# Optimization experiments

Measured on AMD Instinct MI355X. Metric: run time of the kernel, lower is better.

Reference implementation:

```python
import jax, jax.numpy as jnp
import numpy as np

EMBED = 512
HEADS = 8
HEAD_DIM = EMBED // HEADS


def setup_inputs() -> dict:
    key = jax.random.key(0)
    ks = jax.random.split(key, 12)
    B, L, D = 2, 4096, EMBED
    s = 1.0 / np.sqrt(D)  # torch Linear default init range scale (approx, uniform)
    def lin(k):
        kw, kb = jax.random.split(k)
        W = jax.random.uniform(kw, (D, D), jnp.float32, -s, s)
        b = jax.random.uniform(kb, (D,), jnp.float32, -s, s)
        return W, b
    Wq, bq = lin(ks[0])
    Wk, bk = lin(ks[1])
    Wv, bv = lin(ks[2])
    Wo, bo = lin(ks[3])
    query = jax.random.normal(ks[4], (B, L, D), jnp.float32)
    key_t = jax.random.normal(ks[5], (B, L, D), jnp.float32)
    value = jax.random.normal(ks[6], (B, L, D), jnp.float32)
    return {"query": query, "key": key_t, "value": value,
            "Wq": Wq, "bq": bq, "Wk": Wk, "bk": bk,
            "Wv": Wv, "bv": bv, "Wo": Wo, "bo": bo}


def reference(query, key, value, Wq, bq, Wk, bk, Wv, bv, Wo, bo):
    B, L, D = query.shape
    H, Hd = HEADS, HEAD_DIM
    scale = Hd ** -0.5
    # torch nn.Linear: y = x @ W.T + b
    q = (query @ Wq.T + bq).reshape(B, L, H, Hd).transpose(0, 2, 1, 3)   # [B,H,L,Hd]
    k = (key   @ Wk.T + bk).reshape(B, -1, H, Hd).transpose(0, 2, 1, 3)
    v = (value @ Wv.T + bv).reshape(B, -1, H, Hd).transpose(0, 2, 1, 3)
    scores = jnp.einsum('bhqd,bhkd->bhqk', q, k) * scale                  # [B,H,L,L]
    causal = jnp.triu(jnp.ones((L, L), dtype=bool), k=1)                  # True above diag
    neg = jnp.finfo(scores.dtype).min
    scores = jnp.where(causal, neg, scores)
    attn = jax.nn.softmax(scores, axis=-1)
    # dropout is identity in eval mode
    out = jnp.einsum('bhqk,bhkd->bhqd', attn, v)                          # [B,H,L,Hd]
    out = out.transpose(0, 2, 1, 3).reshape(B, L, D)
    return out @ Wo.T + bo, attn
```

## Files before the change

### kernel.cpp

```cpp
#include <hip/hip_runtime.h>
#include <hip/hip_bf16.h>


typedef __attribute__((ext_vector_type(8))) __bf16 bf16x8;
typedef __attribute__((ext_vector_type(4))) __bf16 bf16v4;
typedef __attribute__((ext_vector_type(4))) float f32x4;

constexpr int LL = 4096;
constexpr int DD = 512;
constexpr int HH = 8;
constexpr int HD = 64;
constexpr int BB = 2;
constexpr int BL = BB * LL;
constexpr size_t OUT_ELEMS = (size_t)BB * LL * DD;

static __device__ inline bf16x8 cvt8(const float* p) {
    float4 a = *reinterpret_cast<const float4*>(p);
    float4 b = *reinterpret_cast<const float4*>(p + 4);
    bf16x8 r;
    r[0] = (__bf16)a.x; r[1] = (__bf16)a.y; r[2] = (__bf16)a.z; r[3] = (__bf16)a.w;
    r[4] = (__bf16)b.x; r[5] = (__bf16)b.y; r[6] = (__bf16)b.z; r[7] = (__bf16)b.w;
    return r;
}

static __device__ inline float4 up4(unsigned a, unsigned b) {
    float4 r;
    r.x = __uint_as_float(a << 16);
    r.y = __uint_as_float(a & 0xffff0000u);
    r.z = __uint_as_float(b << 16);
    r.w = __uint_as_float(b & 0xffff0000u);
    return r;
}

__global__ __launch_bounds__(256) void cvt_kernel(
    const float* __restrict__ q, const float* __restrict__ k,
    const float* __restrict__ v, __bf16* __restrict__ o)
{
    constexpr size_t N = (size_t)BL * DD;
    size_t i = ((size_t)blockIdx.x * 256 + threadIdx.x) * 8;
    const float* src = q; size_t j = i;
    if (i >= 2 * N)      { src = v; j = i - 2 * N; }
    else if (i >= N)     { src = k; j = i - N; }
    *reinterpret_cast<bf16x8*>(&o[i]) = cvt8(&src[j]);
}

__global__ __launch_bounds__(256) void qkv_kernel(
    const __bf16* __restrict__ Xb,
    const float* __restrict__ Wq, const float* __restrict__ bq,
    const float* __restrict__ Wk, const float* __restrict__ bk,
    const float* __restrict__ Wv, const float* __restrict__ bv,
    __bf16* __restrict__ Qb, __bf16* __restrict__ Kb, __bf16* __restrict__ Vt)
{
    const int z = blockIdx.z;
    const __bf16* x  = Xb + (size_t)z * BL * DD;
    const float* W   = (z == 0) ? Wq : (z == 1) ? Wk : Wv;
    const float* bia = (z == 0) ? bq : (z == 1) ? bk : bv;

    const int wid = threadIdx.x >> 6;
    const int lane = threadIdx.x & 63;
    const int l15 = lane & 15;
    const int lg  = lane >> 4;

    const int r0 = blockIdx.x * 64;
    const int cb = blockIdx.y;
    const int c0 = cb * 64 + wid * 16;

    f32x4 acc[4] = {};
    for (int k0 = 0; k0 < DD; k0 += 32) {
        bf16x8 bfrag = cvt8(&W[(size_t)(c0 + l15) * DD + k0 + lg * 8]);
#pragma unroll
        for (int mt = 0; mt < 4; ++mt) {
            bf16x8 afrag = *reinterpret_cast<const bf16x8*>(
                &x[(size_t)(r0 + mt * 16 + l15) * DD + k0 + lg * 8]);
            acc[mt] = __builtin_amdgcn_mfma_f32_16x16x32_bf16(afrag, bfrag, acc[mt], 0, 0, 0);
        }
    }

    __shared__ __bf16 T[64][72];
    const float bval = bia[c0 + l15];
#pragma unroll
    for (int mt = 0; mt < 4; ++mt)
#pragma unroll
        for (int i = 0; i < 4; ++i) {
            const float val = acc[mt][i] + bval;
            const int row = mt * 16 + lg * 4 + i;
            const int col = wid * 16 + l15;
            if (z == 2) T[col][row] = (__bf16)val;
            else        T[row][col] = (__bf16)val;
        }
    __syncthreads();

    const int tr  = threadIdx.x >> 2;
    const int seg = threadIdx.x & 3;
    uint4 v0 = *reinterpret_cast<const uint4*>(&T[tr][seg * 16]);
    uint4 v1 = *reinterpret_cast<const uint4*>(&T[tr][seg * 16 + 8]);
    const int b  = r0 >> 12;
    const int l0 = r0 & (LL - 1);
    if (z == 2) {
        __bf16* dst = Vt + ((size_t)(b * HH + cb) * HD + tr) * LL + l0 + seg * 16;
        *reinterpret_cast<uint4*>(dst)     = v0;
        *reinterpret_cast<uint4*>(dst + 8) = v1;
    } else {
        __bf16* base = (z == 0) ? Qb : Kb;
        __bf16* dst = base + ((size_t)(b * HH + cb) * LL + l0 + tr) * HD + seg * 16;
        *reinterpret_cast<uint4*>(dst)     = v0;
        *reinterpret_cast<uint4*>(dst + 8) = v1;
    }
}

__global__ __launch_bounds__(512, 3) void attn_kernel(
    const __bf16* __restrict__ Qb, const __bf16* __restrict__ Kb,
    const __bf16* __restrict__ Vt, __bf16* __restrict__ Ob,
    float* __restrict__ attn_out)
{
    const int bh = blockIdx.x;
    const int qb = 63 - blockIdx.y;

    const int wv   = threadIdx.x >> 6;
    const int wr   = wv & 3;
    const int par  = wv >> 2;
    const int lane = threadIdx.x & 63;
    const int l15  = lane & 15;
    const int lg   = lane >> 4;

    const __bf16* Qh = Qb + (size_t)bh * LL * HD;
    const __bf16* Kh = Kb + (size_t)bh * LL * HD;
    const __bf16* Vh = Vt + (size_t)bh * HD * LL;
    float* A_out = attn_out + (size_t)bh * LL * LL;

    __shared__ __bf16 P[8][16][72];
    __shared__ float rsum[2][64];

    const int q0 = qb * 64 + wr * 16;
    const int qrow = q0 + l15;
    const bf16x8 qf0 = *reinterpret_cast<const bf16x8*>(&Qh[(size_t)(q0 + l15) * HD + lg * 8]);
    const bf16x8 qf1 = *reinterpret_cast<const bf16x8*>(&Qh[(size_t)(q0 + l15) * HD + 32 + lg * 8]);

    const float SC = 0.125f * 1.44269504088896f;

    auto loadK = [&](bf16x8 (&kf)[8], int kb) {
        const __bf16* kp = &Kh[((size_t)kb * 64 + l15) * HD + lg * 8];
#pragma unroll
        for (int kt = 0; kt < 4; ++kt) {
            kf[kt * 2]     = *reinterpret_cast<const bf16x8*>(kp + (size_t)kt * 16 * HD);
            kf[kt * 2 + 1] = *reinterpret_cast<const bf16x8*>(kp + (size_t)kt * 16 * HD + 32);
        }
    };

    float rs = 0.f;
    auto body1 = [&](bf16x8 (&kf)[8], int kb) {
        f32x4 s[4] = {};
#pragma unroll
        for (int kt = 0; kt < 4; ++kt) {
            s[kt] = __builtin_amdgcn_mfma_f32_16x16x32_bf16(kf[kt * 2],     qf0, s[kt], 0, 0, 0);
            s[kt] = __builtin_amdgcn_mfma_f32_16x16x32_bf16(kf[kt * 2 + 1], qf1, s[kt], 0, 0, 0);
        }
        const bool diag = (kb == qb);
#pragma unroll
        for (int kt = 0; kt < 4; ++kt)
#pragma unroll
            for (int i = 0; i < 4; ++i) {
                float e = exp2f(s[kt][i] * SC);
                if (diag && (kb * 64 + kt * 16 + lg * 4 + i) > qrow) e = 0.f;
                rs += e;
            }
    };
    {
        bf16x8 kA[8], kB[8];
        int kb = par;
        bool useA = true;
        if (kb <= qb) loadK(kA, kb);
        for (; kb <= qb; kb += 2) {
            if (useA) { if (kb + 2 <= qb) loadK(kB, kb + 2); body1(kA, kb); }
            else      { if (kb + 2 <= qb) loadK(kA, kb + 2); body1(kB, kb); }
            useA = !useA;
        }
    }
    rs += __shfl_xor(rs, 16, 64);
    rs += __shfl_xor(rs, 32, 64);
    if (lane < 16) rsum[par][wr * 16 + l15] = rs;
    __syncthreads();
    const float llog = -log2f(rsum[0][wr * 16 + l15] + rsum[1][wr * 16 + l15]);

    f32x4 oacc[4] = {};
    const int arow = lane >> 2;
    const int aseg = lane & 3;

    auto body2 = [&](bf16x8 (&kf)[8], int kb) {
        bf16x8 vf[8];
        {
            const __bf16* vp = &Vh[(size_t)l15 * LL + (size_t)kb * 64 + lg * 8];
#pragma unroll
            for (int ht = 0; ht < 4; ++ht) {
                vf[ht * 2]     = *reinterpret_cast<const bf16x8*>(vp + (size_t)ht * 16 * LL);
                vf[ht * 2 + 1] = *reinterpret_cast<const bf16x8*>(vp + (size_t)ht * 16 * LL + 32);
            }
        }
        f32x4 s[4] = {};
#pragma unroll
        for (int kt = 0; kt < 4; ++kt) {
            s[kt] = __builtin_amdgcn_mfma_f32_16x16x32_bf16(kf[kt * 2],     qf0, s[kt], 0, 0, 0);
            s[kt] = __builtin_amdgcn_mfma_f32_16x16x32_bf16(kf[kt * 2 + 1], qf1, s[kt], 0, 0, 0);
        }
        const bool diag = (kb == qb);
#pragma unroll
        for (int kt = 0; kt < 4; ++kt) {
            bf16v4 pk;
#pragma unroll
            for (int i = 0; i < 4; ++i) {
                float e = exp2f(fmaf(s[kt][i], SC, llog));
                if (diag && (kb * 64 + kt * 16 + lg * 4 + i) > qrow) e = 0.f;
                pk[i] = (__bf16)e;
            }
            *reinterpret_cast<bf16v4*>(&P[wv][l15][kt * 16 + lg * 4]) = pk;
        }
        {
            uint4 a0 = *reinterpret_cast<const uint4*>(&P[wv][arow][aseg * 16]);
            uint4 a1 = *reinterpret_cast<const uint4*>(&P[wv][arow][aseg * 16 + 8]);
            float4* dst = reinterpret_cast<float4*>(
                &A_out[(size_t)(q0 + arow) * LL + kb * 64 + aseg * 16]);
            dst[0] = up4(a0.x, a0.y);
            dst[1] = up4(a0.z, a0.w);
            dst[2] = up4(a1.x, a1.y);
            dst[3] = up4(a1.z, a1.w);
        }
        const bf16x8 pa0 = *reinterpret_cast<const bf16x8*>(&P[wv][l15][lg * 8]);
        const bf16x8 pa1 = *reinterpret_cast<const bf16x8*>(&P[wv][l15][32 + lg * 8]);
#pragma unroll
        for (int ht = 0; ht < 4; ++ht) {
            oacc[ht] = __builtin_amdgcn_mfma_f32_16x16x32_bf16(pa0, vf[ht * 2],     oacc[ht], 0, 0, 0);
            oacc[ht] = __builtin_amdgcn_mfma_f32_16x16x32_bf16(pa1, vf[ht * 2 + 1], oacc[ht], 0, 0, 0);
        }
    };
    {
        bf16x8 kA[8], kB[8];
        int kb = par;
        bool useA = true;
        if (kb <= qb) loadK(kA, kb);
        for (; kb <= qb; kb += 2) {
            if (useA) { if (kb + 2 <= qb) loadK(kB, kb + 2); body2(kA, kb); }
            else      { if (kb + 2 <= qb) loadK(kA, kb + 2); body2(kB, kb); }
            useA = !useA;
        }
    }

    if (par == 1) {
#pragma unroll
        for (int ht = 0; ht < 4; ++ht)
#pragma unroll
            for (int i = 0; i < 4; ++i)
                P[wv][lg * 4 + i][ht * 16 + l15] = (__bf16)oacc[ht][i];
    }
    __syncthreads();
    if (par == 0) {
#pragma unroll
        for (int ht = 0; ht < 4; ++ht)
#pragma unroll
            for (int i = 0; i < 4; ++i)
                oacc[ht][i] += (float)P[wv + 4][lg * 4 + i][ht * 16 + l15];
#pragma unroll
        for (int ht = 0; ht < 4; ++ht)
#pragma unroll
            for (int i = 0; i < 4; ++i)
                P[wv][lg * 4 + i][ht * 16 + l15] = (__bf16)oacc[ht][i];
        uint4 o0 = *reinterpret_cast<const uint4*>(&P[wv][arow][aseg * 16]);
        uint4 o1 = *reinterpret_cast<const uint4*>(&P[wv][arow][aseg * 16 + 8]);
        const int b = bh >> 3, h = bh & 7;
        __bf16* dst = Ob + ((size_t)(b * LL + q0 + arow)) * DD + h * HD + aseg * 16;
        *reinterpret_cast<uint4*>(dst)     = o0;
        *reinterpret_cast<uint4*>(dst + 8) = o1;
    }

    {
        const int ztr  = threadIdx.x >> 3;
        const int zseg = threadIdx.x & 7;
        const size_t rowbase = (size_t)(qb * 64 + ztr) * LL;
        const float4 z4 = {0.f, 0.f, 0.f, 0.f};
        for (int c = (qb + 1) * 64 + zseg * 16; c < LL; c += 128) {
            float4* d = reinterpret_cast<float4*>(&A_out[rowbase + c]);
            d[0] = z4; d[1] = z4; d[2] = z4; d[3] = z4;
        }
    }
}

__global__ __launch_bounds__(256) void oproj_kernel(
    const __bf16* __restrict__ Ob, const float* __restrict__ Wo,
    const float* __restrict__ bo, float* __restrict__ out)
{
    const int wid = threadIdx.x >> 6;
    const int lane = threadIdx.x & 63;
    const int l15 = lane & 15;
    const int lg  = lane >> 4;

    const int r0 = blockIdx.x * 64;
    const int c0 = blockIdx.y * 64 + wid * 16;

    f32x4 acc[4] = {};
    for (int k0 = 0; k0 < DD; k0 += 32) {
        bf16x8 bfrag = cvt8(&Wo[(size_t)(c0 + l15) * DD + k0 + lg * 8]);
#pragma unroll
        for (int mt = 0; mt < 4; ++mt) {
            bf16x8 afrag = *reinterpret_cast<const bf16x8*>(
                &Ob[(size_t)(r0 + mt * 16 + l15) * DD + k0 + lg * 8]);
            acc[mt] = __builtin_amdgcn_mfma_f32_16x16x32_bf16(afrag, bfrag, acc[mt], 0, 0, 0);
        }
    }
    const float bval = bo[c0 + l15];
#pragma unroll
    for (int mt = 0; mt < 4; ++mt)
#pragma unroll
        for (int i = 0; i < 4; ++i)
            out[(size_t)(r0 + mt * 16 + lg * 4 + i) * DD + c0 + l15] = acc[mt][i] + bval;
}

extern "C" void kernel_launch(void* const* d_in, const int* in_sizes, int n_in,
                              void* d_out, int out_size, void* d_ws, size_t ws_size,
                              hipStream_t stream) {
    const float* query = (const float*)d_in[0];
    const float* key_t = (const float*)d_in[1];
    const float* value = (const float*)d_in[2];
    const float* Wq = (const float*)d_in[3];
    const float* bq = (const float*)d_in[4];
    const float* Wk = (const float*)d_in[5];
    const float* bk = (const float*)d_in[6];
    const float* Wv = (const float*)d_in[7];
    const float* bv = (const float*)d_in[8];
    const float* Wo = (const float*)d_in[9];
    const float* bo = (const float*)d_in[10];

    float* out  = (float*)d_out;
    float* attn = out + OUT_ELEMS;

    char* ws = (char*)d_ws;
    __bf16* Qb = (__bf16*)(ws);
    __bf16* Kb = (__bf16*)(ws + (size_t)8 * 1024 * 1024);
    __bf16* Vt = (__bf16*)(ws + (size_t)16 * 1024 * 1024);
    __bf16* Ob = (__bf16*)(ws + (size_t)24 * 1024 * 1024);
    __bf16* Xb = (__bf16*)(ws + (size_t)32 * 1024 * 1024);

    cvt_kernel<<<dim3(3 * BL * DD / 8 / 256), 256, 0, stream>>>(query, key_t, value, Xb);
    qkv_kernel<<<dim3(BL / 64, DD / 64, 3), 256, 0, stream>>>(
        Xb, Wq, bq, Wk, bk, Wv, bv, Qb, Kb, Vt);
    attn_kernel<<<dim3(BB * HH, LL / 64), 512, 0, stream>>>(Qb, Kb, Vt, Ob, attn);
    oproj_kernel<<<dim3(BL / 64, DD / 64), 256, 0, stream>>>(Ob, Wo, bo, out);
}
```

Before: 854.0 us.

## Split attention over key chunks into rowsum, main and reduce kernels

Replaces the single attention kernel with a split-K style pipeline. A rowsum kernel computes partial softmax denominators per key chunk, the main kernel computes probabilities and partial P·V per chunk, and a reduce kernel sums the partial outputs. Masked chunks write zeros directly, and attn is now stored from registers in fp32 instead of via bf16 shared memory. The aim is to balance the causal triangle's uneven work across many more blocks. The cost is extra launches, a workspace round trip for partials, and recomputing QK in both passes.

```diff
diff --git a/kernel.cpp b/kernel.cpp
--- a/kernel.cpp
+++ b/kernel.cpp
@@ -13,6 +13,8 @@
 constexpr int BB = 2;
 constexpr int BL = BB * LL;
 constexpr size_t OUT_ELEMS = (size_t)BB * LL * DD;
+constexpr int CH = 16;
+constexpr int NCHUNK = LL / 64 / CH;
 
 static __device__ inline bf16x8 cvt8(const float* p) {
     float4 a = *reinterpret_cast<const float4*>(p);
@@ -20,15 +22,6 @@
     bf16x8 r;
     r[0] = (__bf16)a.x; r[1] = (__bf16)a.y; r[2] = (__bf16)a.z; r[3] = (__bf16)a.w;
     r[4] = (__bf16)b.x; r[5] = (__bf16)b.y; r[6] = (__bf16)b.z; r[7] = (__bf16)b.w;
-    return r;
-}
-
-static __device__ inline float4 up4(unsigned a, unsigned b) {
-    float4 r;
-    r.x = __uint_as_float(a << 16);
-    r.y = __uint_as_float(a & 0xffff0000u);
-    r.z = __uint_as_float(b << 16);
-    r.w = __uint_as_float(b & 0xffff0000u);
     return r;
 }
 
@@ -108,52 +101,40 @@
     }
 }
 
-__global__ __launch_bounds__(512, 3) void attn_kernel(
+__global__ __launch_bounds__(256) void rowsum_kernel(
     const __bf16* __restrict__ Qb, const __bf16* __restrict__ Kb,
-    const __bf16* __restrict__ Vt, __bf16* __restrict__ Ob,
-    float* __restrict__ attn_out)
+    float* __restrict__ rspart)
 {
     const int bh = blockIdx.x;
     const int qb = 63 - blockIdx.y;
+    const int ch = blockIdx.z;
+    if (ch * CH > qb) return;
 
     const int wv   = threadIdx.x >> 6;
-    const int wr   = wv & 3;
-    const int par  = wv >> 2;
     const int lane = threadIdx.x & 63;
     const int l15  = lane & 15;
     const int lg   = lane >> 4;
 
     const __bf16* Qh = Qb + (size_t)bh * LL * HD;
     const __bf16* Kh = Kb + (size_t)bh * LL * HD;
-    const __bf16* Vh = Vt + (size_t)bh * HD * LL;
-    float* A_out = attn_out + (size_t)bh * LL * LL;
-
-    __shared__ __bf16 P[8][16][72];
-    __shared__ float rsum[2][64];
-
-    const int q0 = qb * 64 + wr * 16;
+
+    const int q0 = qb * 64 + wv * 16;
     const int qrow = q0 + l15;
-    const bf16x8 qf0 = *reinterpret_cast<const bf16x8*>(&Qh[(size_t)(q0 + l15) * HD + lg * 8]);
-    const bf16x8 qf1 = *reinterpret_cast<const bf16x8*>(&Qh[(size_t)(q0 + l15) * HD + 32 + lg * 8]);
-
+    const bf16x8 qf0 = *reinterpret_cast<const bf16x8*>(&Qh[(size_t)qrow * HD + lg * 8]);
+    const bf16x8 qf1 = *reinterpret_cast<const bf16x8*>(&Qh[(size_t)qrow * HD + 32 + lg * 8]);
     const float SC = 0.125f * 1.44269504088896f;
 
-    auto loadK = [&](bf16x8 (&kf)[8], int kb) {
-        const __bf16* kp = &Kh[((size_t)kb * 64 + l15) * HD + lg * 8];
+    float rs = 0.f;
+    const int kend = (qb < ch * CH + CH - 1) ? qb : ch * CH + CH - 1;
+    for (int kb = ch * CH; kb <= kend; ++kb) {
+        f32x4 s[4] = {};
 #pragma unroll
         for (int kt = 0; kt < 4; ++kt) {
-            kf[kt * 2]     = *reinterpret_cast<const bf16x8*>(kp + (size_t)kt * 16 * HD);
-            kf[kt * 2 + 1] = *reinterpret_cast<const bf16x8*>(kp + (size_t)kt * 16 * HD + 32);
-        }
-    };
-
-    float rs = 0.f;
-    auto body1 = [&](bf16x8 (&kf)[8], int kb) {
-        f32x4 s[4] = {};
-#pragma unroll
-        for (int kt = 0; kt < 4; ++kt) {
-            s[kt] = __builtin_amdgcn_mfma_f32_16x16x32_bf16(kf[kt * 2],     qf0, s[kt], 0, 0, 0);
-            s[kt] = __builtin_amdgcn_mfma_f32_16x16x32_bf16(kf[kt * 2 + 1], qf1, s[kt], 0, 0, 0);
+            const __bf16* kp = &Kh[(size_t)(kb * 64 + kt * 16 + l15) * HD + lg * 8];
+            const bf16x8 k0 = *reinterpret_cast<const bf16x8*>(kp);
+            const bf16x8 k1 = *reinterpret_cast<const bf16x8*>(kp + 32);
+            s[kt] = __builtin_amdgcn_mfma_f32_16x16x32_bf16(k0, qf0, s[kt], 0, 0, 0);
+            s[kt] = __builtin_amdgcn_mfma_f32_16x16x32_bf16(k1, qf1, s[kt], 0, 0, 0);
         }
         const bool diag = (kb == qb);
 #pragma unroll
@@ -164,31 +145,79 @@
                 if (diag && (kb * 64 + kt * 16 + lg * 4 + i) > qrow) e = 0.f;
                 rs += e;
             }
-    };
-    {
-        bf16x8 kA[8], kB[8];
-        int kb = par;
-        bool useA = true;
-        if (kb <= qb) loadK(kA, kb);
-        for (; kb <= qb; kb += 2) {
-            if (useA) { if (kb + 2 <= qb) loadK(kB, kb + 2); body1(kA, kb); }
-            else      { if (kb + 2 <= qb) loadK(kA, kb + 2); body1(kB, kb); }
-            useA = !useA;
-        }
     }
     rs += __shfl_xor(rs, 16, 64);
     rs += __shfl_xor(rs, 32, 64);
-    if (lane < 16) rsum[par][wr * 16 + l15] = rs;
-    __syncthreads();
-    const float llog = -log2f(rsum[0][wr * 16 + l15] + rsum[1][wr * 16 + l15]);
+    if (lane < 16)
+        rspart[((size_t)bh * LL + qrow) * NCHUNK + ch] = rs;
+}
+
+__global__ __launch_bounds__(256, 4) void attn_main_kernel(
+    const __bf16* __restrict__ Qb, const __bf16* __restrict__ Kb,
+    const __bf16* __restrict__ Vt, const float* __restrict__ rspart,
+    __bf16* __restrict__ opart, float* __restrict__ attn_out)
+{
+    const int bh = blockIdx.x;
+    const int qb = 63 - blockIdx.y;
+    const int ch = blockIdx.z;
+
+    const int wv   = threadIdx.x >> 6;
+    const int lane = threadIdx.x & 63;
+    const int l15  = lane & 15;
+    const int lg   = lane >> 4;
+
+    float* A_out = attn_out + (size_t)bh * LL * LL;
+    const int q0 = qb * 64 + wv * 16;
+    const int qrow = q0 + l15;
+    const int kb0 = ch * CH;
+
+    if (kb0 > qb) {
+        const float4 z4 = {0.f, 0.f, 0.f, 0.f};
+        float4* dst = reinterpret_cast<float4*>(&A_out[(size_t)qrow * LL + kb0 * 64 + lg * 4]);
+        for (int t = 0; t < CH; ++t) {
+#pragma unroll
+            for (int kt = 0; kt < 4; ++kt) dst[kt * 4] = z4;
+            dst += 16;
+        }
+        return;
+    }
+
+    const __bf16* Qh = Qb + (size_t)bh * LL * HD;
+    const __bf16* Kh = Kb + (size_t)bh * LL * HD;
+    const __bf16* Vh = Vt + (size_t)bh * HD * LL;
+
+    __shared__ __bf16 P[4][16][72];
+
+    const bf16x8 qf0 = *reinterpret_cast<const bf16x8*>(&Qh[(size_t)qrow * HD + lg * 8]);
+    const bf16x8 qf1 = *reinterpret_cast<const bf16x8*>(&Qh[(size_t)qrow * HD + 32 + lg * 8]);
+
+    float rsv = 0.f;
+    const int nc = qb >> 4;
+    const float* rp = &rspart[((size_t)bh * LL + qrow) * NCHUNK];
+    for (int c = 0; c <= nc; ++c) rsv += rp[c];
+    const float llog = -log2f(rsv);
+    const float SC = 0.125f * 1.44269504088896f;
 
     f32x4 oacc[4] = {};
-    const int arow = lane >> 2;
-    const int aseg = lane & 3;
-
-    auto body2 = [&](bf16x8 (&kf)[8], int kb) {
-        bf16x8 vf[8];
+
+    for (int t = 0; t < CH; ++t) {
+        const int kb = kb0 + t;
+        if (kb > qb) {
+            const float4 z4 = {0.f, 0.f, 0.f, 0.f};
+            float4* dst = reinterpret_cast<float4*>(
+                &A_out[(size_t)qrow * LL + kb * 64 + lg * 4]);
+#pragma unroll
+            for (int kt = 0; kt < 4; ++kt) dst[kt * 4] = z4;
+            continue;
+        }
+        bf16x8 kf[8], vf[8];
         {
+            const __bf16* kp = &Kh[(size_t)(kb * 64 + l15) * HD + lg * 8];
+#pragma unroll
+            for (int kt = 0; kt < 4; ++kt) {
+                kf[kt * 2]     = *reinterpret_cast<const bf16x8*>(kp + (size_t)kt * 16 * HD);
+                kf[kt * 2 + 1] = *reinterpret_cast<const bf16x8*>(kp + (size_t)kt * 16 * HD + 32);
+            }
             const __bf16* vp = &Vh[(size_t)l15 * LL + (size_t)kb * 64 + lg * 8];
 #pragma unroll
             for (int ht = 0; ht < 4; ++ht) {
@@ -205,24 +234,24 @@
         const bool diag = (kb == qb);
 #pragma unroll
         for (int kt = 0; kt < 4; ++kt) {
+            float e0 = exp2f(fmaf(s[kt][0], SC, llog));
+            float e1 = exp2f(fmaf(s[kt][1], SC, llog));
+            float e2 = exp2f(fmaf(s[kt][2], SC, llog));
+            float e3 = exp2f(fmaf(s[kt][3], SC, llog));
+            if (diag) {
+                const int kc = kb * 64 + kt * 16 + lg * 4;
+                if (kc + 0 > qrow) e0 = 0.f;
+                if (kc + 1 > qrow) e1 = 0.f;
+                if (kc + 2 > qrow) e2 = 0.f;
+                if (kc + 3 > qrow) e3 = 0.f;
+            }
+            float4 ev = {e0, e1, e2, e3};
+            *reinterpret_cast<float4*>(
+                &A_out[(size_t)qrow * LL + kb * 64 + kt * 16 + lg * 4]) = ev;
             bf16v4 pk;
-#pragma unroll
-            for (int i = 0; i < 4; ++i) {
-                float e = exp2f(fmaf(s[kt][i], SC, llog));
-                if (diag && (kb * 64 + kt * 16 + lg * 4 + i) > qrow) e = 0.f;
-                pk[i] = (__bf16)e;
-            }
+            pk[0] = (__bf16)e0; pk[1] = (__bf16)e1;
+            pk[2] = (__bf16)e2; pk[3] = (__bf16)e3;
             *reinterpret_cast<bf16v4*>(&P[wv][l15][kt * 16 + lg * 4]) = pk;
-        }
-        {
-            uint4 a0 = *reinterpret_cast<const uint4*>(&P[wv][arow][aseg * 16]);
-            uint4 a1 = *reinterpret_cast<const uint4*>(&P[wv][arow][aseg * 16 + 8]);
-            float4* dst = reinterpret_cast<float4*>(
-                &A_out[(size_t)(q0 + arow) * LL + kb * 64 + aseg * 16]);
-            dst[0] = up4(a0.x, a0.y);
-            dst[1] = up4(a0.z, a0.w);
-            dst[2] = up4(a1.x, a1.y);
-            dst[3] = up4(a1.z, a1.w);
         }
         const bf16x8 pa0 = *reinterpret_cast<const bf16x8*>(&P[wv][l15][lg * 8]);
         const bf16x8 pa1 = *reinterpret_cast<const bf16x8*>(&P[wv][l15][32 + lg * 8]);
@@ -231,56 +260,49 @@
             oacc[ht] = __builtin_amdgcn_mfma_f32_16x16x32_bf16(pa0, vf[ht * 2],     oacc[ht], 0, 0, 0);
             oacc[ht] = __builtin_amdgcn_mfma_f32_16x16x32_bf16(pa1, vf[ht * 2 + 1], oacc[ht], 0, 0, 0);
         }
-    };
-    {
-        bf16x8 kA[8], kB[8];
-        int kb = par;
-        bool useA = true;
-        if (kb <= qb) loadK(kA, kb);
-        for (; kb <= qb; kb += 2) {
-            if (useA) { if (kb + 2 <= qb) loadK(kB, kb + 2); body2(kA, kb); }
-            else      { if (kb + 2 <= qb) loadK(kA, kb + 2); body2(kB, kb); }
-            useA = !useA;
-        }
-    }
-
-    if (par == 1) {
-#pragma unroll
-        for (int ht = 0; ht < 4; ++ht)
-#pragma unroll
-            for (int i = 0; i < 4; ++i)
-                P[wv][lg * 4 + i][ht * 16 + l15] = (__bf16)oacc[ht][i];
-    }
-    __syncthreads();
-    if (par == 0) {
-#pragma unroll
-        for (int ht = 0; ht < 4; ++ht)
-#pragma unroll
-            for (int i = 0; i < 4; ++i)
-                oacc[ht][i] += (float)P[wv + 4][lg * 4 + i][ht * 16 + l15];
-#pragma unroll
-        for (int ht = 0; ht < 4; ++ht)
-#pragma unroll
-            for (int i = 0; i < 4; ++i)
-                P[wv][lg * 4 + i][ht * 16 + l15] = (__bf16)oacc[ht][i];
-        uint4 o0 = *reinterpret_cast<const uint4*>(&P[wv][arow][aseg * 16]);
-        uint4 o1 = *reinterpret_cast<const uint4*>(&P[wv][arow][aseg * 16 + 8]);
-        const int b = bh >> 3, h = bh & 7;
-        __bf16* dst = Ob + ((size_t)(b * LL + q0 + arow)) * DD + h * HD + aseg * 16;
-        *reinterpret_cast<uint4*>(dst)     = o0;
-        *reinterpret_cast<uint4*>(dst + 8) = o1;
-    }
-
-    {
-        const int ztr  = threadIdx.x >> 3;
-        const int zseg = threadIdx.x & 7;
-        const size_t rowbase = (size_t)(qb * 64 + ztr) * LL;
-        const float4 z4 = {0.f, 0.f, 0.f, 0.f};
-        for (int c = (qb + 1) * 64 + zseg * 16; c < LL; c += 128) {
-            float4* d = reinterpret_cast<float4*>(&A_out[rowbase + c]);
-            d[0] = z4; d[1] = z4; d[2] = z4; d[3] = z4;
-        }
-    }
+    }
+
+#pragma unroll
+    for (int ht = 0; ht < 4; ++ht)
+#pragma unroll
+        for (int i = 0; i < 4; ++i)
+            P[wv][lg * 4 + i][ht * 16 + l15] = (__bf16)oacc[ht][i];
+    const int arow = lane >> 2;
+    const int aseg = lane & 3;
+    uint4 o0 = *reinterpret_cast<const uint4*>(&P[wv][arow][aseg * 16]);
+    uint4 o1 = *reinterpret_cast<const uint4*>(&P[wv][arow][aseg * 16 + 8]);
+    __bf16* dst = opart + ((size_t)((bh * 64 + qb) * NCHUNK + ch)) * 4096
+                + (wv * 16 + arow) * 64 + aseg * 16;
+    *reinterpret_cast<uint4*>(dst)     = o0;
+    *reinterpret_cast<uint4*>(dst + 8) = o1;
+}
+
+__global__ __launch_bounds__(256) void oreduce_kernel(
+    const __bf16* __restrict__ opart, __bf16* __restrict__ Ob)
+{
+    const int bh = blockIdx.x;
+    const int qb = blockIdx.y;
+    const int nc = qb >> 4;
+    const __bf16* src = opart + ((size_t)(bh * 64 + qb) * NCHUNK) * 4096;
+    const int t = threadIdx.x;
+
+    float acc[16] = {};
+    for (int c = 0; c <= nc; ++c) {
+        bf16x8 a = *reinterpret_cast<const bf16x8*>(&src[(size_t)c * 4096 + t * 16]);
+        bf16x8 b = *reinterpret_cast<const bf16x8*>(&src[(size_t)c * 4096 + t * 16 + 8]);
+#pragma unroll
+        for (int j = 0; j < 8; ++j) { acc[j] += (float)a[j]; acc[8 + j] += (float)b[j]; }
+    }
+    bf16x8 r0, r1;
+#pragma unroll
+    for (int j = 0; j < 8; ++j) { r0[j] = (__bf16)acc[j]; r1[j] = (__bf16)acc[8 + j]; }
+
+    const int qr  = t >> 2;
+    const int hd0 = (t & 3) * 16;
+    const int b = bh >> 3, h = bh & 7;
+    __bf16* dst = Ob + ((size_t)(b * LL + qb * 64 + qr)) * DD + h * HD + hd0;
+    *reinterpret_cast<bf16x8*>(dst)     = r0;
+    *reinterpret_cast<bf16x8*>(dst + 8) = r1;
 }
 
 __global__ __launch_bounds__(256) void oproj_kernel(
@@ -332,15 +354,20 @@
     float* attn = out + OUT_ELEMS;
 
     char* ws = (char*)d_ws;
-    __bf16* Qb = (__bf16*)(ws);
-    __bf16* Kb = (__bf16*)(ws + (size_t)8 * 1024 * 1024);
-    __bf16* Vt = (__bf16*)(ws + (size_t)16 * 1024 * 1024);
-    __bf16* Ob = (__bf16*)(ws + (size_t)24 * 1024 * 1024);
-    __bf16* Xb = (__bf16*)(ws + (size_t)32 * 1024 * 1024);
+    __bf16* Qb     = (__bf16*)(ws);
+    __bf16* Kb     = (__bf16*)(ws +  8388608);
+    __bf16* Vt     = (__bf16*)(ws + 16777216);
+    __bf16* Ob     = (__bf16*)(ws + 25165824);
+    float*  rspart = (float*) (ws + 33554432);
+    __bf16* Xb     = (__bf16*)(ws + 34603008);
+    __bf16* opart  = (__bf16*)(ws + 34603008);
 
     cvt_kernel<<<dim3(3 * BL * DD / 8 / 256), 256, 0, stream>>>(query, key_t, value, Xb);
     qkv_kernel<<<dim3(BL / 64, DD / 64, 3), 256, 0, stream>>>(
         Xb, Wq, bq, Wk, bk, Wv, bv, Qb, Kb, Vt);
-    attn_kernel<<<dim3(BB * HH, LL / 64), 512, 0, stream>>>(Qb, Kb, Vt, Ob, attn);
+    rowsum_kernel<<<dim3(BB * HH, LL / 64, NCHUNK), 256, 0, stream>>>(Qb, Kb, rspart);
+    attn_main_kernel<<<dim3(BB * HH, LL / 64, NCHUNK), 256, 0, stream>>>(
+        Qb, Kb, Vt, rspart, opart, attn);
+    oreduce_kernel<<<dim3(BB * HH, LL / 64), 256, 0, stream>>>(opart, Ob);
     oproj_kernel<<<dim3(BL / 64, DD / 64), 256, 0, stream>>>(Ob, Wo, bo, out);
 }
```

Result: faster. 786.8 us (-7.9%).
